# Optimization experiments

Hardware: AMD Instinct MI355X
Metric: run time of the kernel (lower is better)

Reference implementation:

```python
import jax, jax.numpy as jnp
import numpy as np

TEMPERATURE = 0.5


def setup_inputs() -> dict:
    key = jax.random.key(0)
    k1, k2 = jax.random.split(key)
    N, D = 4096, 256
    emb_i = jax.random.normal(k1, (N, D), dtype=jnp.float32)
    emb_j = jax.random.normal(k2, (N, D), dtype=jnp.float32)
    return {"emb_i": emb_i, "emb_j": emb_j, "batch_size": N}


def reference(emb_i, emb_j, batch_size):
    N = batch_size
    # L2-normalize each embedding row (F.normalize eps=1e-12)
    def l2n(x):
        return x / jnp.maximum(jnp.linalg.norm(x, axis=1, keepdims=True), 1e-12)
    reps = jnp.concatenate([l2n(emb_i), l2n(emb_j)], axis=0)  # [2N, D]
    # cosine similarity of normalized vectors == dot product
    logits = (reps @ reps.T) / TEMPERATURE                    # [2N, 2N]
    twoN = 2 * N
    # denominator excludes only the self term k != i (stable logsumexp)
    diag_mask = jnp.eye(twoN, dtype=bool)
    masked = jnp.where(diag_mask, -jnp.inf, logits)
    log_denom = jax.nn.logsumexp(masked, axis=1)              # [2N]
    # positive pair for row i is (i+N) mod 2N
    idx = jnp.arange(twoN)
    pos = logits[idx, (idx + N) % twoN]                       # [2N]
    # loss = 1/(2N) * sum_i -log(exp(pos_i)/denom_i)
    return jnp.mean(log_denom - pos)
```

## Files before the change

### kernel.cpp

```cpp
#include <hip/hip_runtime.h>

typedef short short8 __attribute__((ext_vector_type(8)));
typedef float f32x4  __attribute__((ext_vector_type(4)));

#define TWO_N 8192
#define NHALF 4096
#define DDIM  256

__device__ __forceinline__ float b2f(unsigned short u) {
    return __uint_as_float(((unsigned int)u) << 16);
}
__device__ __forceinline__ unsigned short f2b(float f) {
    unsigned int u = __float_as_uint(f);
    u += 0x7fffu + ((u >> 16) & 1u);
    return (unsigned short)(u >> 16);
}

__device__ __forceinline__ int probe_is_f32(const void* p, int lane) {
    unsigned int u = ((const unsigned int*)p)[lane];
    float lowv = __uint_as_float(u << 16);
    int crazy = !(fabsf(lowv) <= 1024.0f);
    return __ballot(crazy) != 0ull;
}

typedef __attribute__((address_space(1))) const unsigned int guint_t;
typedef __attribute__((address_space(3))) unsigned int luint_t;
__device__ __forceinline__ void gl_lds16(const unsigned short* g, unsigned short* l) {
    __builtin_amdgcn_global_load_lds((guint_t*)(const void*)g, (luint_t*)(void*)l, 16, 0, 0);
}

__global__ __launch_bounds__(256) void k_norm(const void* __restrict__ ei,
                                              const void* __restrict__ ej,
                                              unsigned short* __restrict__ reps) {
    int row  = (blockIdx.x * 256 + threadIdx.x) >> 6;
    int lane = threadIdx.x & 63;
    int isf  = probe_is_f32(ei, lane);
    int first = (row < NHALF);
    int r     = first ? row : row - NHALF;
    float x0, x1, x2, x3;
    if (isf) {
        const float* s = (first ? (const float*)ei : (const float*)ej) + (size_t)r * DDIM;
        float4 v = ((const float4*)s)[lane];
        x0 = v.x; x1 = v.y; x2 = v.z; x3 = v.w;
    } else {
        const unsigned short* s =
            (first ? (const unsigned short*)ei : (const unsigned short*)ej) + (size_t)r * DDIM;
        ushort4 v = ((const ushort4*)s)[lane];
        x0 = b2f(v.x); x1 = b2f(v.y); x2 = b2f(v.z); x3 = b2f(v.w);
    }
    float ss = x0 * x0 + x1 * x1 + x2 * x2 + x3 * x3;
    for (int off = 32; off > 0; off >>= 1) ss += __shfl_xor(ss, off);
    float inv = 1.0f / fmaxf(sqrtf(ss), 1e-12f);
    ushort4 o;
    o.x = f2b(x0 * inv); o.y = f2b(x1 * inv);
    o.z = f2b(x2 * inv); o.w = f2b(x3 * inv);
    ((ushort4*)(reps + (size_t)row * DDIM))[lane] = o;
}

__global__ __launch_bounds__(256) void k_main(const unsigned short* __restrict__ R,
                                              float* __restrict__ S_part,
                                              float* __restrict__ pos) {
    __shared__ __align__(16) unsigned short As[128 * 64];
    __shared__ __align__(16) unsigned short Bs[128 * 64];

    int b = blockIdx.x;
    int rb = (int)((129.0f - sqrtf(16641.0f - 8.0f * (float)b)) * 0.5f);
    if (rb > 63) rb = 63;
    while ((129 * (rb + 1) - (rb + 1) * (rb + 1)) / 2 <= b) ++rb;
    while ((129 * rb - rb * rb) / 2 > b) --rb;
    int cb = rb + (b - (129 * rb - rb * rb) / 2);

    const int tid  = threadIdx.x;
    const int wave = tid >> 6;
    const int lane = tid & 63;
    const int quad = lane >> 4;
    const int l16  = lane & 15;
    const int wr   = (wave >> 1) * 64;
    const int wc   = (wave & 1) * 64;
    const int r8   = lane >> 3;
    const int c8   = (lane & 7) ^ r8;

    f32x4 acc[4][4];
#pragma unroll
    for (int r = 0; r < 4; ++r)
#pragma unroll
        for (int c = 0; c < 4; ++c) {
            acc[r][c][0] = 0.0f; acc[r][c][1] = 0.0f;
            acc[r][c][2] = 0.0f; acc[r][c][3] = 0.0f;
        }

    for (int kc = 0; kc < 4; ++kc) {
        __syncthreads();
#pragma unroll
        for (int t = 0; t < 4; ++t) {
            int u = wave * 4 + t;
            const unsigned short* ga =
                R + (size_t)(rb * 128 + u * 8 + r8) * DDIM + kc * 64 + c8 * 8;
            const unsigned short* gb =
                R + (size_t)(cb * 128 + u * 8 + r8) * DDIM + kc * 64 + c8 * 8;
            gl_lds16(ga, &As[u * 512]);
            gl_lds16(gb, &Bs[u * 512]);
        }
        __syncthreads();

#pragma unroll
        for (int kk = 0; kk < 2; ++kk) {
            short8 afr[4], bfr[4];
            int q = kk * 4 + quad;
            int sl = q ^ (l16 & 7);
#pragma unroll
            for (int r = 0; r < 4; ++r)
                afr[r] = *(const short8*)(&As[(wr + r * 16 + l16) * 64 + sl * 8]);
#pragma unroll
            for (int c = 0; c < 4; ++c)
                bfr[c] = *(const short8*)(&Bs[(wc + c * 16 + l16) * 64 + sl * 8]);
#pragma unroll
            for (int r = 0; r < 4; ++r)
#pragma unroll
                for (int c = 0; c < 4; ++c)
                    acc[r][c] = __builtin_amdgcn_mfma_f32_16x16x32_bf16(
                        afr[r], bfr[c], acc[r][c], 0, 0, 0);
        }
    }

    float col_acc[4] = {0.0f, 0.0f, 0.0f, 0.0f};
#pragma unroll
    for (int r = 0; r < 4; ++r)
#pragma unroll
        for (int j = 0; j < 4; ++j) {
            float s = 0.0f;
#pragma unroll
            for (int c = 0; c < 4; ++c) {
                float e = __expf(fmaf(acc[r][c][j], 2.0f, -2.0f));
                s += e;
                col_acc[c] += e;
            }
            s += __shfl_xor(s, 1);
            s += __shfl_xor(s, 2);
            s += __shfl_xor(s, 4);
            s += __shfl_xor(s, 8);
            if (l16 == 0) {
                int row = rb * 128 + wr + r * 16 + quad * 4 + j;
                S_part[(size_t)(2 * cb + (wave & 1)) * TWO_N + row] = s;
            }
        }
    if (rb != cb) {
#pragma unroll
        for (int c = 0; c < 4; ++c) {
            float s = col_acc[c];
            s += __shfl_xor(s, 16);
            s += __shfl_xor(s, 32);
            if (lane < 16) {
                int row = cb * 128 + wc + c * 16 + lane;
                S_part[(size_t)(2 * rb + (wave >> 1)) * TWO_N + row] = s;
            }
        }
    }
    if (cb == rb + 32 && wr == wc) {
#pragma unroll
        for (int r = 0; r < 4; ++r)
#pragma unroll
            for (int j = 0; j < 4; ++j)
                if (quad * 4 + j == l16)
                    pos[rb * 128 + wr + r * 16 + l16] = 2.0f * acc[r][r][j];
    }
}

__global__ __launch_bounds__(256) void k_rows(const float* __restrict__ S_part,
                                              const float* __restrict__ pos,
                                              float* __restrict__ t_row) {
    int row = blockIdx.x * 256 + threadIdx.x;
    float s = 0.0f;
    for (int c = 0; c < 128; ++c) s += S_part[(size_t)c * TWO_N + row];
    float p = (row < NHALF) ? pos[row] : pos[row - NHALF];
    t_row[row] = 2.0f + logf(s - 1.0f) - p;
}

__global__ __launch_bounds__(1024) void k_fin(const float* __restrict__ t_row,
                                              unsigned int* __restrict__ out) {
    int tid = threadIdx.x;
    float local = 0.0f;
    for (int i = tid; i < TWO_N; i += 1024) local += t_row[i];
    __shared__ float red[16];
    for (int off = 32; off > 0; off >>= 1) local += __shfl_xor(local, off);
    if ((tid & 63) == 0) red[tid >> 6] = local;
    __syncthreads();
    if (tid == 0) {
        float v = 0.0f;
        for (int w = 0; w < 16; ++w) v += red[w];
        float L = v / 8192.0f;
        unsigned int bb = (unsigned int)f2b(L);
        out[0] = (bb << 16) | bb;
    }
}

extern "C" void kernel_launch(void* const* d_in, const int* in_sizes, int n_in,
                              void* d_out, int out_size, void* d_ws, size_t ws_size,
                              hipStream_t stream) {
    (void)in_sizes; (void)n_in; (void)out_size; (void)ws_size;
    const void* ei = d_in[0];
    const void* ej = d_in[1];
    char* ws = (char*)d_ws;

    float*          pos    = (float*)(ws);
    float*          t_row  = (float*)(ws + 16384);
    unsigned short* reps   = (unsigned short*)(ws + 49152);
    float*          S_part = (float*)(ws + 4243456);

    k_norm<<<2048, 256, 0, stream>>>(ei, ej, reps);
    k_main<<<2080, 256, 0, stream>>>(reps, S_part, pos);
    k_rows<<<32,   256, 0, stream>>>(S_part, pos, t_row);
    k_fin <<<1,   1024, 0, stream>>>(t_row, (unsigned int*)d_out);
}
```

Baseline: 110.1 us.

## Keep A fragments in registers, double-buffer B tiles, and split row/column partial sums

Each wave now loads its 32 rows of A straight from global memory into registers for the full K=256, so A is no longer staged through LDS. Only B goes through LDS, and it is double-buffered so the next K chunk is prefetched during the MFMAs, with one barrier per chunk instead of two. The wave layout changes from 2x2 (64x64) to 4x1 (32x128), and the partial sums go to separate S_row and S_col buffers that k_rows reads only over their valid triangular ranges, so it reads less data. In exchange, register pressure rises (af holds 16 short8 values and acc holds 16 f32x4), which may lower occupancy, and the A loads from global are uncoalesced row-strided reads.

Result: slower. 233.6 us (+112.2%).

```diff
diff --git a/kernel.cpp b/kernel.cpp
--- a/kernel.cpp
+++ b/kernel.cpp
@@ -58,10 +58,10 @@
 }
 
 __global__ __launch_bounds__(256) void k_main(const unsigned short* __restrict__ R,
-                                              float* __restrict__ S_part,
+                                              float* __restrict__ S_row,
+                                              float* __restrict__ S_col,
                                               float* __restrict__ pos) {
-    __shared__ __align__(16) unsigned short As[128 * 64];
-    __shared__ __align__(16) unsigned short Bs[128 * 64];
+    __shared__ __align__(16) unsigned short Bs[2][128 * 64];
 
     int b = blockIdx.x;
     int rb = (int)((129.0f - sqrtf(16641.0f - 8.0f * (float)b)) * 0.5f);
@@ -71,67 +71,76 @@
     int cb = rb + (b - (129 * rb - rb * rb) / 2);
 
     const int tid  = threadIdx.x;
-    const int wave = tid >> 6;
+    const int w    = tid >> 6;
     const int lane = tid & 63;
     const int quad = lane >> 4;
     const int l16  = lane & 15;
-    const int wr   = (wave >> 1) * 64;
-    const int wc   = (wave & 1) * 64;
     const int r8   = lane >> 3;
     const int c8   = (lane & 7) ^ r8;
 
-    f32x4 acc[4][4];
-#pragma unroll
-    for (int r = 0; r < 4; ++r)
-#pragma unroll
-        for (int c = 0; c < 4; ++c) {
-            acc[r][c][0] = 0.0f; acc[r][c][1] = 0.0f;
-            acc[r][c][2] = 0.0f; acc[r][c][3] = 0.0f;
-        }
+    short8 af[2][8];
+#pragma unroll
+    for (int rt = 0; rt < 2; ++rt) {
+        const unsigned short* base =
+            R + (size_t)(rb * 128 + w * 32 + rt * 16 + l16) * DDIM + quad * 8;
+#pragma unroll
+        for (int kt = 0; kt < 8; ++kt)
+            af[rt][kt] = *(const short8*)(base + kt * 32);
+    }
+
+    f32x4 acc[2][8];
+#pragma unroll
+    for (int rt = 0; rt < 2; ++rt)
+#pragma unroll
+        for (int c = 0; c < 8; ++c) {
+            acc[rt][c][0] = 0.0f; acc[rt][c][1] = 0.0f;
+            acc[rt][c][2] = 0.0f; acc[rt][c][3] = 0.0f;
+        }
+
+#pragma unroll
+    for (int t = 0; t < 4; ++t) {
+        int u = w * 4 + t;
+        gl_lds16(R + (size_t)(cb * 128 + u * 8 + r8) * DDIM + c8 * 8,
+                 &Bs[0][u * 512]);
+    }
 
     for (int kc = 0; kc < 4; ++kc) {
         __syncthreads();
-#pragma unroll
-        for (int t = 0; t < 4; ++t) {
-            int u = wave * 4 + t;
-            const unsigned short* ga =
-                R + (size_t)(rb * 128 + u * 8 + r8) * DDIM + kc * 64 + c8 * 8;
-            const unsigned short* gb =
-                R + (size_t)(cb * 128 + u * 8 + r8) * DDIM + kc * 64 + c8 * 8;
-            gl_lds16(ga, &As[u * 512]);
-            gl_lds16(gb, &Bs[u * 512]);
-        }
-        __syncthreads();
-
+        if (kc < 3) {
+#pragma unroll
+            for (int t = 0; t < 4; ++t) {
+                int u = w * 4 + t;
+                gl_lds16(R + (size_t)(cb * 128 + u * 8 + r8) * DDIM + (kc + 1) * 64 + c8 * 8,
+                         &Bs[(kc + 1) & 1][u * 512]);
+            }
+        }
+        const unsigned short* bsrc = Bs[kc & 1];
 #pragma unroll
         for (int kk = 0; kk < 2; ++kk) {
-            short8 afr[4], bfr[4];
-            int q = kk * 4 + quad;
+            int q  = kk * 4 + quad;
             int sl = q ^ (l16 & 7);
-#pragma unroll
-            for (int r = 0; r < 4; ++r)
-                afr[r] = *(const short8*)(&As[(wr + r * 16 + l16) * 64 + sl * 8]);
-#pragma unroll
-            for (int c = 0; c < 4; ++c)
-                bfr[c] = *(const short8*)(&Bs[(wc + c * 16 + l16) * 64 + sl * 8]);
-#pragma unroll
-            for (int r = 0; r < 4; ++r)
-#pragma unroll
-                for (int c = 0; c < 4; ++c)
-                    acc[r][c] = __builtin_amdgcn_mfma_f32_16x16x32_bf16(
-                        afr[r], bfr[c], acc[r][c], 0, 0, 0);
-        }
-    }
-
-    float col_acc[4] = {0.0f, 0.0f, 0.0f, 0.0f};
-#pragma unroll
-    for (int r = 0; r < 4; ++r)
+            short8 bfr[8];
+#pragma unroll
+            for (int c = 0; c < 8; ++c)
+                bfr[c] = *(const short8*)(&bsrc[(c * 16 + l16) * 64 + sl * 8]);
+#pragma unroll
+            for (int rt = 0; rt < 2; ++rt)
+#pragma unroll
+                for (int c = 0; c < 8; ++c)
+                    acc[rt][c] = __builtin_amdgcn_mfma_f32_16x16x32_bf16(
+                        af[rt][kc * 2 + kk], bfr[c], acc[rt][c], 0, 0, 0);
+        }
+    }
+
+    float col_acc[8] = {0.f, 0.f, 0.f, 0.f, 0.f, 0.f, 0.f, 0.f};
+#pragma unroll
+    for (int rt = 0; rt < 2; ++rt)
 #pragma unroll
         for (int j = 0; j < 4; ++j) {
             float s = 0.0f;
 #pragma unroll
-            for (int c = 0; c < 4; ++c) {
-                float e = __expf(fmaf(acc[r][c][j], 2.0f, -2.0f));
+            for (int c = 0; c < 8; ++c) {
+                float e = __expf(fmaf(acc[rt][c][j], 2.0f, -2.0f));
                 s += e;
                 col_acc[c] += e;
             }
@@ -140,38 +149,42 @@
             s += __shfl_xor(s, 4);
             s += __shfl_xor(s, 8);
             if (l16 == 0) {
-                int row = rb * 128 + wr + r * 16 + quad * 4 + j;
-                S_part[(size_t)(2 * cb + (wave & 1)) * TWO_N + row] = s;
+                int row = rb * 128 + w * 32 + rt * 16 + quad * 4 + j;
+                S_row[(size_t)cb * TWO_N + row] = s;
             }
         }
     if (rb != cb) {
 #pragma unroll
-        for (int c = 0; c < 4; ++c) {
+        for (int c = 0; c < 8; ++c) {
             float s = col_acc[c];
             s += __shfl_xor(s, 16);
             s += __shfl_xor(s, 32);
             if (lane < 16) {
-                int row = cb * 128 + wc + c * 16 + lane;
-                S_part[(size_t)(2 * rb + (wave >> 1)) * TWO_N + row] = s;
-            }
-        }
-    }
-    if (cb == rb + 32 && wr == wc) {
-#pragma unroll
-        for (int r = 0; r < 4; ++r)
+                int col = cb * 128 + c * 16 + lane;
+                S_col[(size_t)(rb * 4 + w) * TWO_N + col] = s;
+            }
+        }
+    }
+    if (cb == rb + 32) {
+#pragma unroll
+        for (int rt = 0; rt < 2; ++rt)
 #pragma unroll
             for (int j = 0; j < 4; ++j)
-                if (quad * 4 + j == l16)
-                    pos[rb * 128 + wr + r * 16 + l16] = 2.0f * acc[r][r][j];
-    }
-}
-
-__global__ __launch_bounds__(256) void k_rows(const float* __restrict__ S_part,
+                if (l16 == quad * 4 + j)
+                    pos[rb * 128 + w * 32 + rt * 16 + l16] =
+                        2.0f * acc[rt][w * 2 + rt][j];
+    }
+}
+
+__global__ __launch_bounds__(256) void k_rows(const float* __restrict__ S_row,
+                                              const float* __restrict__ S_col,
                                               const float* __restrict__ pos,
                                               float* __restrict__ t_row) {
     int row = blockIdx.x * 256 + threadIdx.x;
+    int t   = row >> 7;
     float s = 0.0f;
-    for (int c = 0; c < 128; ++c) s += S_part[(size_t)c * TWO_N + row];
+    for (int c = t; c < 64; ++c)  s += S_row[(size_t)c * TWO_N + row];
+    for (int q = 0; q < 4 * t; ++q) s += S_col[(size_t)q * TWO_N + row];
     float p = (row < NHALF) ? pos[row] : pos[row - NHALF];
     t_row[row] = 2.0f + logf(s - 1.0f) - p;
 }
@@ -187,7 +200,7 @@
     __syncthreads();
     if (tid == 0) {
         float v = 0.0f;
-        for (int w = 0; w < 16; ++w) v += red[w];
+        for (int wv = 0; wv < 16; ++wv) v += red[wv];
         float L = v / 8192.0f;
         unsigned int bb = (unsigned int)f2b(L);
         out[0] = (bb << 16) | bb;
@@ -202,13 +215,14 @@
     const void* ej = d_in[1];
     char* ws = (char*)d_ws;
 
-    float*          pos    = (float*)(ws);
-    float*          t_row  = (float*)(ws + 16384);
-    unsigned short* reps   = (unsigned short*)(ws + 49152);
-    float*          S_part = (float*)(ws + 4243456);
+    float*          pos   = (float*)(ws);
+    float*          t_row = (float*)(ws + 16384);
+    unsigned short* reps  = (unsigned short*)(ws + 49152);
+    float*          S_row = (float*)(ws + 4243456);
+    float*          S_col = (float*)(ws + 6340608);
 
     k_norm<<<2048, 256, 0, stream>>>(ei, ej, reps);
-    k_main<<<2080, 256, 0, stream>>>(reps, S_part, pos);
-    k_rows<<<32,   256, 0, stream>>>(S_part, pos, t_row);
+    k_main<<<2080, 256, 0, stream>>>(reps, S_row, S_col, pos);
+    k_rows<<<32,   256, 0, stream>>>(S_row, S_col, pos, t_row);
     k_fin <<<1,   1024, 0, stream>>>(t_row, (unsigned int*)d_out);
 }
```
